# Kernel optimization log

Hardware: AMD Instinct MI355X
Metric: run time of the kernel (lower is better)

## Reference

```python
import jax, jax.numpy as jnp
import numpy as np

N = 100000   # nodes
E = 1600000  # edges (avg degree 16)
D = 32       # feature / hidden dim


def setup_inputs() -> dict:
    key = jax.random.key(0)
    k_x, k_e, kq, kk, kv, ko = jax.random.split(key, 6)
    s = 1.0 / np.sqrt(D).astype(np.float32)
    x = jax.random.normal(k_x, (N, D), dtype=jnp.float32)
    edge_index = jax.random.randint(k_e, (2, E), 0, N, dtype=jnp.int64)
    Wq = jax.random.normal(kq, (D, D), dtype=jnp.float32) * s
    Wk = jax.random.normal(kk, (D, D), dtype=jnp.float32) * s
    Wv = jax.random.normal(kv, (D, D), dtype=jnp.float32) * s
    Wo = jax.random.normal(ko, (D, D), dtype=jnp.float32) * s
    return {"x": x, "edge_index": edge_index, "Wq": Wq, "Wk": Wk, "Wv": Wv, "Wo": Wo}


def reference(x, edge_index, Wq, Wk, Wv, Wo):
    sender, receiver = edge_index[0], edge_index[1]
    n = x.shape[0]
    scale = x.shape[1] ** -0.5  # hidden_dim == D
    Q = x @ Wq  # [N, D]
    K = x @ Wk
    V = x @ Wv
    # per-edge attention scores
    scores = jnp.sum(Q[receiver] * K[sender], axis=1) * scale  # [E]
    # numerically-stable segment softmax over incoming edges of each receiver
    smax = jax.ops.segment_max(scores, receiver, num_segments=n)  # [N]
    alpha = jnp.exp(scores - smax[receiver])  # [E]
    Z = jax.ops.segment_sum(alpha, receiver, num_segments=n)  # [N]
    alpha = alpha / (Z[receiver] + 1e-6)
    # weighted aggregation of sender values
    out = jax.ops.segment_sum(alpha[:, None] * V[sender], receiver, num_segments=n)  # [N, D]
    return x + out @ Wo
```

## Files before the change

kernel.cpp:

```cpp
#include <hip/hip_runtime.h>

#define DIM 32
#define RCR 256
#define NCMAX 1024
#define PBLK 256
#define SUBCAP 48
#define REGSZ (PBLK * SUBCAP)
#define CAPC 5248

__device__ __forceinline__ float b2f(ushort h) {
    union { float f; unsigned u; } u; u.u = ((unsigned)h) << 16; return u.f;
}
__device__ __forceinline__ float h2f(ushort u) {
    _Float16 h; __builtin_memcpy(&h, &u, 2); return (float)h;
}
__device__ __forceinline__ ushort f2h(float f) {
    _Float16 h = (_Float16)f; ushort u; __builtin_memcpy(&u, &h, 2); return u;
}
__device__ __forceinline__ int clampN(int v, int n) {
    return v < 0 ? 0 : (v >= n ? n - 1 : v);
}
__device__ __forceinline__ int load_idx(const int* __restrict__ idx, size_t pos,
                                        int mode, int n) {
    int v = mode ? idx[2 * pos] : idx[pos];
    return clampN(v, n);
}
__device__ __forceinline__ float load_f(const void* p, size_t i, int bf) {
    return bf ? b2f(((const ushort*)p)[i]) : ((const float*)p)[i];
}

typedef _Float16 half2v __attribute__((ext_vector_type(2)));
__device__ __forceinline__ float dot2(unsigned a, unsigned b, float c) {
#if __has_builtin(__builtin_amdgcn_fdot2)
    half2v ha, hb;
    __builtin_memcpy(&ha, &a, 4); __builtin_memcpy(&hb, &b, 4);
    return __builtin_amdgcn_fdot2(ha, hb, c, false);
#else
    return fmaf(h2f((ushort)(a >> 16)), h2f((ushort)(b >> 16)),
                fmaf(h2f((ushort)a), h2f((ushort)b), c));
#endif
}

union K1Smem {
    struct { float sW[3][DIM * DIM]; float sx[32][36]; } g;
    struct { int h[NCMAX]; } place;
};

__global__ void __launch_bounds__(256)
qkv_place_kernel(const void* __restrict__ x_, const int* __restrict__ idx,
                 const void* __restrict__ Wq_, const void* __restrict__ Wk_,
                 const void* __restrict__ Wv_, int N, int E, int nc,
                 ushort* __restrict__ Q, ushort* __restrict__ KV,
                 unsigned* __restrict__ bedges, int* __restrict__ hcnt) {
    __shared__ K1Smem sm;
    __shared__ int sBf, sMode;

    const int tid = threadIdx.x;
    if (tid < 64) {
        int e = (((const ushort*)x_)[2 * tid] >> 7) & 0xFF;
        unsigned long long bb = __ballot(e >= 100 && e <= 135);
        unsigned long long mm = __ballot(idx[2 * tid + 1] != 0);
        if (tid == 0) { sBf = (__popcll(bb) >= 56); sMode = (mm == 0ULL); }
    }
    __syncthreads();
    const int bf = sBf, mode = sMode;

    if (blockIdx.x < PBLK) {
        const int pb = blockIdx.x;
        for (int i = tid; i < nc; i += 256) sm.place.h[i] = 0;
        __syncthreads();
        const int per = (E + PBLK - 1) / PBLK;
        const int e0 = pb * per;
        const int e1 = min(e0 + per, E);
        for (int e = e0 + tid; e < e1; e += 256) {
            const int r = load_idx(idx, (size_t)E + e, mode, N);
            const int s = load_idx(idx, (size_t)e, mode, N);
            const int reg = r >> 8;
            const int rl  = r & (RCR - 1);
            const int p = atomicAdd(&sm.place.h[reg], 1);
            if (p < SUBCAP)
                bedges[(size_t)reg * REGSZ + pb * SUBCAP + p] =
                    (unsigned)s | ((unsigned)rl << 17);
        }
        __syncthreads();
        for (int i = tid; i < nc; i += 256)
            hcnt[i * PBLK + pb] = min(sm.place.h[i], SUBCAP);
        return;
    }

    for (int i = tid; i < DIM * DIM; i += 256) {
        sm.g.sW[0][i] = load_f(Wq_, i, bf);
        sm.g.sW[1][i] = load_f(Wk_, i, bf);
        sm.g.sW[2][i] = load_f(Wv_, i, bf);
    }
    const int base = (blockIdx.x - PBLK) * 32;
    for (int i = tid; i < 32 * 8; i += 256) {
        const int r  = i >> 3;
        const int c4 = (i & 7) << 2;
        const int row = base + r;
        float4 v; v.x = v.y = v.z = v.w = 0.f;
        if (row < N) {
            if (!bf) {
                v = *(const float4*)((const float*)x_ + (size_t)row * DIM + c4);
            } else {
                const ushort4 u =
                    *(const ushort4*)((const ushort*)x_ + (size_t)row * DIM + c4);
                v.x = b2f(u.x); v.y = b2f(u.y); v.z = b2f(u.z); v.w = b2f(u.w);
            }
        }
        *(float4*)&sm.g.sx[r][c4] = v;
    }
    __syncthreads();

    const int lr  = tid >> 3;
    const int d4  = (tid & 7) << 2;
    const int row = base + lr;
    if (row >= N) return;

    float aq[4] = {0.f, 0.f, 0.f, 0.f};
    float ak[4] = {0.f, 0.f, 0.f, 0.f};
    float av[4] = {0.f, 0.f, 0.f, 0.f};
#pragma unroll
    for (int k0 = 0; k0 < DIM; k0 += 4) {
        const float4 xq = *(const float4*)&sm.g.sx[lr][k0];
        const float xs[4] = {xq.x, xq.y, xq.z, xq.w};
#pragma unroll
        for (int kk = 0; kk < 4; ++kk) {
            const float xv = xs[kk];
            const float4 wq = *(const float4*)&sm.g.sW[0][(k0 + kk) * DIM + d4];
            const float4 wk = *(const float4*)&sm.g.sW[1][(k0 + kk) * DIM + d4];
            const float4 wv = *(const float4*)&sm.g.sW[2][(k0 + kk) * DIM + d4];
            aq[0] = fmaf(xv, wq.x, aq[0]); aq[1] = fmaf(xv, wq.y, aq[1]);
            aq[2] = fmaf(xv, wq.z, aq[2]); aq[3] = fmaf(xv, wq.w, aq[3]);
            ak[0] = fmaf(xv, wk.x, ak[0]); ak[1] = fmaf(xv, wk.y, ak[1]);
            ak[2] = fmaf(xv, wk.z, ak[2]); ak[3] = fmaf(xv, wk.w, ak[3]);
            av[0] = fmaf(xv, wv.x, av[0]); av[1] = fmaf(xv, wv.y, av[1]);
            av[2] = fmaf(xv, wv.z, av[2]); av[3] = fmaf(xv, wv.w, av[3]);
        }
    }
    const float sc = 0.17677669529663687f;
    ushort4 t;
    t.x = f2h(aq[0] * sc); t.y = f2h(aq[1] * sc);
    t.z = f2h(aq[2] * sc); t.w = f2h(aq[3] * sc);
    *(ushort4*)&Q[(size_t)row * DIM + d4] = t;
    t.x = f2h(ak[0]); t.y = f2h(ak[1]); t.z = f2h(ak[2]); t.w = f2h(ak[3]);
    *(ushort4*)&KV[(size_t)row * 64 + d4] = t;
    t.x = f2h(av[0]); t.y = f2h(av[1]); t.z = f2h(av[2]); t.w = f2h(av[3]);
    *(ushort4*)&KV[(size_t)row * 64 + 32 + d4] = t;
}

__global__ void __launch_bounds__(512)
rsort_kernel(unsigned* __restrict__ bedges, const int* __restrict__ hcnt,
             int* __restrict__ rbase, int* __restrict__ rcount, int N) {
    __shared__ unsigned eL[CAPC];
    __shared__ int cnt[RCR];
    __shared__ int fills[PBLK];
    __shared__ int cbase[PBLK];
    __shared__ int wsum[4];

    const int tid = threadIdx.x;
    const int c = blockIdx.x;
    const size_t s0 = (size_t)c * REGSZ;
    const int lane = tid & 63, w = tid >> 6;

    if (tid < RCR) cnt[tid] = 0;
    if (tid < PBLK) fills[tid] = hcnt[c * PBLK + tid];
    __syncthreads();

    int fv = 0, fx = 0;
    if (tid < PBLK) {
        fv = fills[tid]; fx = fv;
#pragma unroll
        for (int o = 1; o < 64; o <<= 1) {
            int t = __shfl_up(fx, o); if (lane >= o) fx += t;
        }
        if (lane == 63) wsum[w] = fx;
    }
    __syncthreads();
    if (tid == 0) {
        int a = 0;
#pragma unroll
        for (int k = 0; k < 4; ++k) { int t = wsum[k]; wsum[k] = a; a += t; }
    }
    __syncthreads();
    if (tid < PBLK) cbase[tid] = fx - fv + wsum[w];
    __syncthreads();
    const int nTot = cbase[PBLK - 1] + fills[PBLK - 1];

    for (int j = tid; j < REGSZ / 4; j += 512) {
        const int cell = j / (SUBCAP / 4);
        const int q0   = (j - cell * (SUBCAP / 4)) * 4;
        const int fc   = fills[cell];
        if (q0 < fc) {
            const uint4 e4 = *(const uint4*)&bedges[s0 + (size_t)j * 4];
            const int base = cbase[cell] + q0;
            if (base < CAPC) {
                eL[base] = e4.x;
                atomicAdd(&cnt[(e4.x >> 17) & (RCR - 1)], 1);
            }
            if (q0 + 1 < fc && base + 1 < CAPC) {
                eL[base + 1] = e4.y;
                atomicAdd(&cnt[(e4.y >> 17) & (RCR - 1)], 1);
            }
            if (q0 + 2 < fc && base + 2 < CAPC) {
                eL[base + 2] = e4.z;
                atomicAdd(&cnt[(e4.z >> 17) & (RCR - 1)], 1);
            }
            if (q0 + 3 < fc && base + 3 < CAPC) {
                eL[base + 3] = e4.w;
                atomicAdd(&cnt[(e4.w >> 17) & (RCR - 1)], 1);
            }
        }
    }
    __syncthreads();

    const int v = (tid < RCR) ? cnt[tid] : 0;
    int x = v;
    if (tid < RCR) {
#pragma unroll
        for (int o = 1; o < 64; o <<= 1) {
            int t = __shfl_up(x, o); if (lane >= o) x += t;
        }
        if (lane == 63) wsum[w] = x;
    }
    __syncthreads();
    if (tid == 0) {
        int a = 0;
#pragma unroll
        for (int k = 0; k < 4; ++k) { int t = wsum[k]; wsum[k] = a; a += t; }
    }
    __syncthreads();
    int excl = 0;
    if (tid < RCR) {
        excl = x - v + wsum[w];
        rbase[c * RCR + tid]  = (int)s0 + excl;
        rcount[c * RCR + tid] = v;
    }
    __syncthreads();
    if (tid < RCR) cnt[tid] = excl;
    __syncthreads();

    const int m = min(nTot, CAPC);
    for (int i = tid; i < m; i += 512) {
        const unsigned e = eL[i];
        const int p = atomicAdd(&cnt[(e >> 17) & (RCR - 1)], 1);
        bedges[s0 + p] = e & 0x1FFFF;
    }
}

__global__ void __launch_bounds__(256)
agg_kernel(const ushort* __restrict__ Q, const ushort* __restrict__ KV,
           const unsigned* __restrict__ bedges, const int* __restrict__ rbase,
           const int* __restrict__ rcount, const void* __restrict__ x_,
           const void* __restrict__ Wo_, int N, float* __restrict__ out) {
    __shared__ float sWo[DIM * DIM];
    __shared__ float accS[32][DIM + 1];
    __shared__ float Zs[32];
    __shared__ unsigned sQ[32 * 16];
    __shared__ int sBf;

    const int tid = threadIdx.x;
    if (tid < 64) {
        int e = (((const ushort*)x_)[2 * tid] >> 7) & 0xFF;
        unsigned long long bb = __ballot(e >= 100 && e <= 135);
        if (tid == 0) sBf = (__popcll(bb) >= 56);
    }
    const int r0 = blockIdx.x * 32;
    const int nr = min(32, N - r0);
    __syncthreads();
    const int bf = sBf;

    for (int i = tid; i < DIM * DIM; i += 256) sWo[i] = load_f(Wo_, i, bf);
    for (int i = tid; i < nr * 16; i += 256)
        sQ[i] = ((const unsigned*)(Q + (size_t)r0 * DIM))[i];
    __syncthreads();

    const int w    = tid >> 6;
    const int lane = tid & 63;
    const int i8   = lane >> 3;
    const int j    = lane & 7;

    for (int t = w; t < nr; t += 8) {
        const int rlA = t;
        const int rlB = t + 4;
        const bool hasB = (rlB < nr);

        const int degA = rcount[r0 + rlA];
        const int o0A  = rbase[r0 + rlA];
        const int degB = hasB ? rcount[r0 + rlB] : 0;
        const int o0B  = hasB ? rbase[r0 + rlB] : o0A;

        const unsigned qA01 = sQ[rlA * 16 + j * 2];
        const unsigned qA23 = sQ[rlA * 16 + j * 2 + 1];
        const unsigned qB01 = sQ[(rlB & 31) * 16 + j * 2];
        const unsigned qB23 = sQ[(rlB & 31) * 16 + j * 2 + 1];

        float axA = 0.f, ayA = 0.f, azA = 0.f, awA = 0.f, zsA = 0.f;
        float axB = 0.f, ayB = 0.f, azB = 0.f, awB = 0.f, zsB = 0.f;

        const int chA = (degA + 7) >> 3;
        const int chB = (degB + 7) >> 3;
        const int cmax = max(chA, chB);
        const int dmA = max(degA - 1, 0);
        const int dmB = max(degB - 1, 0);

        for (int cc = 0; cc < cmax; cc += 2) {
            const int c0 = cc * 8 + i8;
            const int c1 = c0 + 8;
            const bool okA0 = (c0 < degA), okA1 = (c1 < degA);
            const bool okB0 = (c0 < degB), okB1 = (c1 < degB);

            const int sA0 = (int)bedges[o0A + (okA0 ? c0 : dmA)];
            const int sA1 = (int)bedges[o0A + (okA1 ? c1 : dmA)];
            const int sB0 = (int)bedges[o0B + (okB0 ? c0 : dmB)];
            const int sB1 = (int)bedges[o0B + (okB1 ? c1 : dmB)];

            const ushort* pA0 = KV + (size_t)sA0 * 64;
            const ushort* pA1 = KV + (size_t)sA1 * 64;
            const ushort* pB0 = KV + (size_t)sB0 * 64;
            const ushort* pB1 = KV + (size_t)sB1 * 64;

            const uint2 kA0 = *(const uint2*)(pA0 + j * 4);
            const uint2 vA0 = *(const uint2*)(pA0 + 32 + j * 4);
            const uint2 kA1 = *(const uint2*)(pA1 + j * 4);
            const uint2 vA1 = *(const uint2*)(pA1 + 32 + j * 4);
            const uint2 kB0 = *(const uint2*)(pB0 + j * 4);
            const uint2 vB0 = *(const uint2*)(pB0 + 32 + j * 4);
            const uint2 kB1 = *(const uint2*)(pB1 + j * 4);
            const uint2 vB1 = *(const uint2*)(pB1 + 32 + j * 4);

            float pA  = dot2(kA0.y, qA23, dot2(kA0.x, qA01, 0.f));
            float pAx = dot2(kA1.y, qA23, dot2(kA1.x, qA01, 0.f));
            float pB  = dot2(kB0.y, qB23, dot2(kB0.x, qB01, 0.f));
            float pBx = dot2(kB1.y, qB23, dot2(kB1.x, qB01, 0.f));

            pA  += __shfl_xor(pA, 1);   pAx += __shfl_xor(pAx, 1);
            pB  += __shfl_xor(pB, 1);   pBx += __shfl_xor(pBx, 1);
            pA  += __shfl_xor(pA, 2);   pAx += __shfl_xor(pAx, 2);
            pB  += __shfl_xor(pB, 2);   pBx += __shfl_xor(pBx, 2);
            pA  += __shfl_xor(pA, 4);   pAx += __shfl_xor(pAx, 4);
            pB  += __shfl_xor(pB, 4);   pBx += __shfl_xor(pBx, 4);

            pA  = fminf(fmaxf(pA,  -60.f), 60.f);
            pAx = fminf(fmaxf(pAx, -60.f), 60.f);
            pB  = fminf(fmaxf(pB,  -60.f), 60.f);
            pBx = fminf(fmaxf(pBx, -60.f), 60.f);
            const float aA0 = okA0 ? __expf(pA)  : 0.f;
            const float aA1 = okA1 ? __expf(pAx) : 0.f;
            const float aB0 = okB0 ? __expf(pB)  : 0.f;
            const float aB1 = okB1 ? __expf(pBx) : 0.f;

            axA = fmaf(h2f((ushort)vA0.x), aA0, axA);
            ayA = fmaf(h2f((ushort)(vA0.x >> 16)), aA0, ayA);
            azA = fmaf(h2f((ushort)vA0.y), aA0, azA);
            awA = fmaf(h2f((ushort)(vA0.y >> 16)), aA0, awA);
            axA = fmaf(h2f((ushort)vA1.x), aA1, axA);
            ayA = fmaf(h2f((ushort)(vA1.x >> 16)), aA1, ayA);
            azA = fmaf(h2f((ushort)vA1.y), aA1, azA);
            awA = fmaf(h2f((ushort)(vA1.y >> 16)), aA1, awA);
            zsA += aA0 + aA1;

            axB = fmaf(h2f((ushort)vB0.x), aB0, axB);
            ayB = fmaf(h2f((ushort)(vB0.x >> 16)), aB0, ayB);
            azB = fmaf(h2f((ushort)vB0.y), aB0, azB);
            awB = fmaf(h2f((ushort)(vB0.y >> 16)), aB0, awB);
            axB = fmaf(h2f((ushort)vB1.x), aB1, axB);
            ayB = fmaf(h2f((ushort)(vB1.x >> 16)), aB1, ayB);
            azB = fmaf(h2f((ushort)vB1.y), aB1, azB);
            awB = fmaf(h2f((ushort)(vB1.y >> 16)), aB1, awB);
            zsB += aB0 + aB1;
        }

#pragma unroll
        for (int o = 8; o < 64; o <<= 1) {
            axA += __shfl_xor(axA, o); ayA += __shfl_xor(ayA, o);
            azA += __shfl_xor(azA, o); awA += __shfl_xor(awA, o);
            zsA += __shfl_xor(zsA, o);
            axB += __shfl_xor(axB, o); ayB += __shfl_xor(ayB, o);
            azB += __shfl_xor(azB, o); awB += __shfl_xor(awB, o);
            zsB += __shfl_xor(zsB, o);
        }
        if (i8 == 0) {
            float* arA = accS[rlA];
            arA[j * 4 + 0] = axA; arA[j * 4 + 1] = ayA;
            arA[j * 4 + 2] = azA; arA[j * 4 + 3] = awA;
            if (j == 0) Zs[rlA] = zsA;
            if (hasB) {
                float* arB = accS[rlB];
                arB[j * 4 + 0] = axB; arB[j * 4 + 1] = ayB;
                arB[j * 4 + 2] = azB; arB[j * 4 + 3] = awB;
                if (j == 0) Zs[rlB] = zsB;
            }
        }
    }
    __syncthreads();

    const int lr = tid >> 5;
    const int d  = tid & 31;
#pragma unroll
    for (int it = 0; it < 4; ++it) {
        const int rl = it * 8 + lr;
        if (rl < nr) {
            const float inv = 1.f / (Zs[rl] + 1e-6f);
            float o = 0.f;
#pragma unroll
            for (int k = 0; k < DIM; ++k) o += accS[rl][k] * sWo[k * DIM + d];
            const size_t oi = (size_t)(r0 + rl) * DIM + d;
            out[oi] = load_f(x_, oi, bf) + inv * o;
        }
    }
}

extern "C" void kernel_launch(void* const* d_in, const int* in_sizes, int n_in,
                              void* d_out, int out_size, void* d_ws, size_t ws_size,
                              hipStream_t stream) {
    const void* x   = d_in[0];
    const int*  idx = (const int*)d_in[1];
    const void* Wq  = d_in[2];
    const void* Wk  = d_in[3];
    const void* Wv  = d_in[4];
    const void* Wo  = d_in[5];
    float* out = (float*)d_out;

    const int N = in_sizes[0] / DIM;
    const int E = in_sizes[1] / 2;
    const int nc = (N + RCR - 1) / RCR;
    const size_t N32 = (size_t)N * DIM;

    ushort*   Q      = (ushort*)d_ws;
    ushort*   KV     = Q + N32;
    unsigned* bedges = (unsigned*)(KV + (size_t)N * 64);
    int*      hcnt   = (int*)(bedges + (size_t)nc * REGSZ);
    int*      rbase  = hcnt + (size_t)nc * PBLK;
    int*      rcount = rbase + (size_t)nc * RCR;

    const int gemm_blocks = (N + 31) / 32;
    qkv_place_kernel<<<PBLK + gemm_blocks, 256, 0, stream>>>(
        x, idx, Wq, Wk, Wv, N, E, nc, Q, KV, bedges, hcnt);

    rsort_kernel<<<nc, 512, 0, stream>>>(bedges, hcnt, rbase, rcount, N);

    agg_kernel<<<(N + 31) / 32, 256, 0, stream>>>(Q, KV, bedges, rbase,
                                                  rcount, x, Wo, N, out);
}
```

Measured before the change: 177.1 us.

## Gather 16-byte K/V chunks with four lanes per edge, four rows per wave

Restructures the per-receiver gather loop. Each edge now uses 4 lanes doing 16-byte loads instead of 8 lanes doing 8-byte loads, so 16 edges are processed per wave step. Each wave handles four receiver rows at once over two passes instead of two. This widens the memory transactions and raises the number of independent gathers in flight. In exchange it adds more registers for the 32 accumulators plus the q vectors, and the final cross-lane reduction grows from 10 to 36 values per step.

```diff
diff --git a/kernel.cpp b/kernel.cpp
--- a/kernel.cpp
+++ b/kernel.cpp
@@ -277,119 +277,89 @@
 
     const int w    = tid >> 6;
     const int lane = tid & 63;
-    const int i8   = lane >> 3;
-    const int j    = lane & 7;
-
-    for (int t = w; t < nr; t += 8) {
-        const int rlA = t;
-        const int rlB = t + 4;
-        const bool hasB = (rlB < nr);
-
-        const int degA = rcount[r0 + rlA];
-        const int o0A  = rbase[r0 + rlA];
-        const int degB = hasB ? rcount[r0 + rlB] : 0;
-        const int o0B  = hasB ? rbase[r0 + rlB] : o0A;
-
-        const unsigned qA01 = sQ[rlA * 16 + j * 2];
-        const unsigned qA23 = sQ[rlA * 16 + j * 2 + 1];
-        const unsigned qB01 = sQ[(rlB & 31) * 16 + j * 2];
-        const unsigned qB23 = sQ[(rlB & 31) * 16 + j * 2 + 1];
-
-        float axA = 0.f, ayA = 0.f, azA = 0.f, awA = 0.f, zsA = 0.f;
-        float axB = 0.f, ayB = 0.f, azB = 0.f, awB = 0.f, zsB = 0.f;
-
-        const int chA = (degA + 7) >> 3;
-        const int chB = (degB + 7) >> 3;
-        const int cmax = max(chA, chB);
-        const int dmA = max(degA - 1, 0);
-        const int dmB = max(degB - 1, 0);
-
-        for (int cc = 0; cc < cmax; cc += 2) {
-            const int c0 = cc * 8 + i8;
-            const int c1 = c0 + 8;
-            const bool okA0 = (c0 < degA), okA1 = (c1 < degA);
-            const bool okB0 = (c0 < degB), okB1 = (c1 < degB);
-
-            const int sA0 = (int)bedges[o0A + (okA0 ? c0 : dmA)];
-            const int sA1 = (int)bedges[o0A + (okA1 ? c1 : dmA)];
-            const int sB0 = (int)bedges[o0B + (okB0 ? c0 : dmB)];
-            const int sB1 = (int)bedges[o0B + (okB1 ? c1 : dmB)];
-
-            const ushort* pA0 = KV + (size_t)sA0 * 64;
-            const ushort* pA1 = KV + (size_t)sA1 * 64;
-            const ushort* pB0 = KV + (size_t)sB0 * 64;
-            const ushort* pB1 = KV + (size_t)sB1 * 64;
-
-            const uint2 kA0 = *(const uint2*)(pA0 + j * 4);
-            const uint2 vA0 = *(const uint2*)(pA0 + 32 + j * 4);
-            const uint2 kA1 = *(const uint2*)(pA1 + j * 4);
-            const uint2 vA1 = *(const uint2*)(pA1 + 32 + j * 4);
-            const uint2 kB0 = *(const uint2*)(pB0 + j * 4);
-            const uint2 vB0 = *(const uint2*)(pB0 + 32 + j * 4);
-            const uint2 kB1 = *(const uint2*)(pB1 + j * 4);
-            const uint2 vB1 = *(const uint2*)(pB1 + 32 + j * 4);
-
-            float pA  = dot2(kA0.y, qA23, dot2(kA0.x, qA01, 0.f));
-            float pAx = dot2(kA1.y, qA23, dot2(kA1.x, qA01, 0.f));
-            float pB  = dot2(kB0.y, qB23, dot2(kB0.x, qB01, 0.f));
-            float pBx = dot2(kB1.y, qB23, dot2(kB1.x, qB01, 0.f));
-
-            pA  += __shfl_xor(pA, 1);   pAx += __shfl_xor(pAx, 1);
-            pB  += __shfl_xor(pB, 1);   pBx += __shfl_xor(pBx, 1);
-            pA  += __shfl_xor(pA, 2);   pAx += __shfl_xor(pAx, 2);
-            pB  += __shfl_xor(pB, 2);   pBx += __shfl_xor(pBx, 2);
-            pA  += __shfl_xor(pA, 4);   pAx += __shfl_xor(pAx, 4);
-            pB  += __shfl_xor(pB, 4);   pBx += __shfl_xor(pBx, 4);
-
-            pA  = fminf(fmaxf(pA,  -60.f), 60.f);
-            pAx = fminf(fmaxf(pAx, -60.f), 60.f);
-            pB  = fminf(fmaxf(pB,  -60.f), 60.f);
-            pBx = fminf(fmaxf(pBx, -60.f), 60.f);
-            const float aA0 = okA0 ? __expf(pA)  : 0.f;
-            const float aA1 = okA1 ? __expf(pAx) : 0.f;
-            const float aB0 = okB0 ? __expf(pB)  : 0.f;
-            const float aB1 = okB1 ? __expf(pBx) : 0.f;
-
-            axA = fmaf(h2f((ushort)vA0.x), aA0, axA);
-            ayA = fmaf(h2f((ushort)(vA0.x >> 16)), aA0, ayA);
-            azA = fmaf(h2f((ushort)vA0.y), aA0, azA);
-            awA = fmaf(h2f((ushort)(vA0.y >> 16)), aA0, awA);
-            axA = fmaf(h2f((ushort)vA1.x), aA1, axA);
-            ayA = fmaf(h2f((ushort)(vA1.x >> 16)), aA1, ayA);
-            azA = fmaf(h2f((ushort)vA1.y), aA1, azA);
-            awA = fmaf(h2f((ushort)(vA1.y >> 16)), aA1, awA);
-            zsA += aA0 + aA1;
-
-            axB = fmaf(h2f((ushort)vB0.x), aB0, axB);
-            ayB = fmaf(h2f((ushort)(vB0.x >> 16)), aB0, ayB);
-            azB = fmaf(h2f((ushort)vB0.y), aB0, azB);
-            awB = fmaf(h2f((ushort)(vB0.y >> 16)), aB0, awB);
-            axB = fmaf(h2f((ushort)vB1.x), aB1, axB);
-            ayB = fmaf(h2f((ushort)(vB1.x >> 16)), aB1, ayB);
-            azB = fmaf(h2f((ushort)vB1.y), aB1, azB);
-            awB = fmaf(h2f((ushort)(vB1.y >> 16)), aB1, awB);
-            zsB += aB0 + aB1;
-        }
-
-#pragma unroll
-        for (int o = 8; o < 64; o <<= 1) {
-            axA += __shfl_xor(axA, o); ayA += __shfl_xor(ayA, o);
-            azA += __shfl_xor(azA, o); awA += __shfl_xor(awA, o);
-            zsA += __shfl_xor(zsA, o);
-            axB += __shfl_xor(axB, o); ayB += __shfl_xor(ayB, o);
-            azB += __shfl_xor(azB, o); awB += __shfl_xor(awB, o);
-            zsB += __shfl_xor(zsB, o);
-        }
-        if (i8 == 0) {
-            float* arA = accS[rlA];
-            arA[j * 4 + 0] = axA; arA[j * 4 + 1] = ayA;
-            arA[j * 4 + 2] = azA; arA[j * 4 + 3] = awA;
-            if (j == 0) Zs[rlA] = zsA;
-            if (hasB) {
-                float* arB = accS[rlB];
-                arB[j * 4 + 0] = axB; arB[j * 4 + 1] = ayB;
-                arB[j * 4 + 2] = azB; arB[j * 4 + 3] = awB;
-                if (j == 0) Zs[rlB] = zsB;
+    const int i16  = lane >> 2;
+    const int j    = lane & 3;
+
+    for (int qq = 0; qq < 2; ++qq) {
+        int rl[4], deg[4], o0[4], dm[4];
+        uint4 qw[4];
+        float acc[4][8];
+        float zs[4];
+#pragma unroll
+        for (int k = 0; k < 4; ++k) {
+            rl[k] = w + 4 * k + 16 * qq;
+            const bool valid = rl[k] < nr;
+            deg[k] = valid ? rcount[r0 + rl[k]] : 0;
+            o0[k]  = valid ? rbase[r0 + rl[k]] : rbase[r0];
+            dm[k]  = max(deg[k] - 1, 0);
+            qw[k]  = ((const uint4*)(sQ + (rl[k] & 31) * 16))[j];
+#pragma unroll
+            for (int i = 0; i < 8; ++i) acc[k][i] = 0.f;
+            zs[k] = 0.f;
+        }
+        const int cmax = max(max((deg[0] + 15) >> 4, (deg[1] + 15) >> 4),
+                             max((deg[2] + 15) >> 4, (deg[3] + 15) >> 4));
+
+        for (int cc = 0; cc < cmax; ++cc) {
+            const int c0 = cc * 16 + i16;
+            bool ok[4]; int sx[4];
+#pragma unroll
+            for (int k = 0; k < 4; ++k) {
+                ok[k] = c0 < deg[k];
+                sx[k] = (int)bedges[o0[k] + (ok[k] ? c0 : dm[k])];
+            }
+            uint4 kw[4], vw[4];
+#pragma unroll
+            for (int k = 0; k < 4; ++k) {
+                const ushort* p = KV + (size_t)sx[k] * 64;
+                kw[k] = *(const uint4*)(p + j * 8);
+                vw[k] = *(const uint4*)(p + 32 + j * 8);
+            }
+            float a[4];
+#pragma unroll
+            for (int k = 0; k < 4; ++k) {
+                float p = dot2(kw[k].x, qw[k].x, 0.f);
+                p = dot2(kw[k].y, qw[k].y, p);
+                p = dot2(kw[k].z, qw[k].z, p);
+                p = dot2(kw[k].w, qw[k].w, p);
+                p += __shfl_xor(p, 1);
+                p += __shfl_xor(p, 2);
+                p = fminf(fmaxf(p, -60.f), 60.f);
+                a[k] = ok[k] ? __expf(p) : 0.f;
+            }
+#pragma unroll
+            for (int k = 0; k < 4; ++k) {
+                acc[k][0] = fmaf(h2f((ushort)vw[k].x),         a[k], acc[k][0]);
+                acc[k][1] = fmaf(h2f((ushort)(vw[k].x >> 16)), a[k], acc[k][1]);
+                acc[k][2] = fmaf(h2f((ushort)vw[k].y),         a[k], acc[k][2]);
+                acc[k][3] = fmaf(h2f((ushort)(vw[k].y >> 16)), a[k], acc[k][3]);
+                acc[k][4] = fmaf(h2f((ushort)vw[k].z),         a[k], acc[k][4]);
+                acc[k][5] = fmaf(h2f((ushort)(vw[k].z >> 16)), a[k], acc[k][5]);
+                acc[k][6] = fmaf(h2f((ushort)vw[k].w),         a[k], acc[k][6]);
+                acc[k][7] = fmaf(h2f((ushort)(vw[k].w >> 16)), a[k], acc[k][7]);
+                zs[k] += a[k];
+            }
+        }
+
+#pragma unroll
+        for (int o = 4; o < 64; o <<= 1) {
+#pragma unroll
+            for (int k = 0; k < 4; ++k) {
+#pragma unroll
+                for (int i = 0; i < 8; ++i)
+                    acc[k][i] += __shfl_xor(acc[k][i], o);
+                zs[k] += __shfl_xor(zs[k], o);
+            }
+        }
+        if (i16 == 0) {
+#pragma unroll
+            for (int k = 0; k < 4; ++k) {
+                if (rl[k] < nr) {
+#pragma unroll
+                    for (int i = 0; i < 8; ++i)
+                        accS[rl[k]][j * 8 + i] = acc[k][i];
+                    if (j == 0) Zs[rl[k]] = zs[k];
+                }
             }
         }
     }
```

Measured after the change: 198.0 us. +11.8%, slower.

## Move QKV GEMM from place kernel into rsort kernel and vectorize index loads

Applied to the files above, without the earlier changes.

Splits edge placement into its own kernel with 512 threads, loading two edges per iteration through vectorized int2/int4 loads. The QKV projection moves out of the placement kernel and runs alongside the per-region sort in a combined launch, using 64-row tiles at 512 threads. The aim is to shorten the placement phase and fill the otherwise under-occupied sort launch (only a few hundred blocks) with GEMM work. The cost is a larger shared-memory union that may limit occupancy, plus a different block mix per launch.

```diff
diff --git a/kernel.cpp b/kernel.cpp
--- a/kernel.cpp
+++ b/kernel.cpp
@@ -41,62 +41,205 @@
 #endif
 }
 
-union K1Smem {
-    struct { float sW[3][DIM * DIM]; float sx[32][36]; } g;
-    struct { int h[NCMAX]; } place;
-};
-
-__global__ void __launch_bounds__(256)
-qkv_place_kernel(const void* __restrict__ x_, const int* __restrict__ idx,
-                 const void* __restrict__ Wq_, const void* __restrict__ Wk_,
-                 const void* __restrict__ Wv_, int N, int E, int nc,
-                 ushort* __restrict__ Q, ushort* __restrict__ KV,
-                 unsigned* __restrict__ bedges, int* __restrict__ hcnt) {
-    __shared__ K1Smem sm;
-    __shared__ int sBf, sMode;
+__global__ void __launch_bounds__(512)
+place_kernel(const int* __restrict__ idx, int N, int E, int nc,
+             unsigned* __restrict__ bedges, int* __restrict__ hcnt) {
+    __shared__ int sh[NCMAX];
+    __shared__ int sMode;
 
     const int tid = threadIdx.x;
     if (tid < 64) {
-        int e = (((const ushort*)x_)[2 * tid] >> 7) & 0xFF;
-        unsigned long long bb = __ballot(e >= 100 && e <= 135);
         unsigned long long mm = __ballot(idx[2 * tid + 1] != 0);
-        if (tid == 0) { sBf = (__popcll(bb) >= 56); sMode = (mm == 0ULL); }
-    }
-    __syncthreads();
-    const int bf = sBf, mode = sMode;
-
-    if (blockIdx.x < PBLK) {
-        const int pb = blockIdx.x;
-        for (int i = tid; i < nc; i += 256) sm.place.h[i] = 0;
-        __syncthreads();
+        if (tid == 0) sMode = (mm == 0ULL);
+    }
+    for (int i = tid; i < nc; i += 512) sh[i] = 0;
+    __syncthreads();
+    const int mode = sMode;
+    const int pb = blockIdx.x;
+
+    if ((E & 1) == 0) {
+        const int pairs = E >> 1;
+        const int per = (pairs + PBLK - 1) / PBLK;
+        const int p0 = pb * per;
+        const int p1 = min(p0 + per, pairs);
+        for (int p = p0 + tid; p < p1; p += 512) {
+            int sa, sb, ra, rb;
+            if (mode) {
+                const int4 sv = *(const int4*)&idx[(size_t)4 * p];
+                const int4 rv = *(const int4*)&idx[2 * (size_t)E + (size_t)4 * p];
+                sa = sv.x; sb = sv.z; ra = rv.x; rb = rv.z;
+            } else {
+                const int2 sv = *(const int2*)&idx[(size_t)2 * p];
+                const int2 rv = *(const int2*)&idx[(size_t)E + (size_t)2 * p];
+                sa = sv.x; sb = sv.y; ra = rv.x; rb = rv.y;
+            }
+            sa = clampN(sa, N); sb = clampN(sb, N);
+            ra = clampN(ra, N); rb = clampN(rb, N);
+            const int ga = ra >> 8, la = ra & (RCR - 1);
+            const int gb = rb >> 8, lb = rb & (RCR - 1);
+            const int pa = atomicAdd(&sh[ga], 1);
+            if (pa < SUBCAP)
+                bedges[(size_t)ga * REGSZ + pb * SUBCAP + pa] =
+                    (unsigned)sa | ((unsigned)la << 17);
+            const int pb2 = atomicAdd(&sh[gb], 1);
+            if (pb2 < SUBCAP)
+                bedges[(size_t)gb * REGSZ + pb * SUBCAP + pb2] =
+                    (unsigned)sb | ((unsigned)lb << 17);
+        }
+    } else {
         const int per = (E + PBLK - 1) / PBLK;
         const int e0 = pb * per;
         const int e1 = min(e0 + per, E);
-        for (int e = e0 + tid; e < e1; e += 256) {
+        for (int e = e0 + tid; e < e1; e += 512) {
             const int r = load_idx(idx, (size_t)E + e, mode, N);
             const int s = load_idx(idx, (size_t)e, mode, N);
             const int reg = r >> 8;
             const int rl  = r & (RCR - 1);
-            const int p = atomicAdd(&sm.place.h[reg], 1);
+            const int p = atomicAdd(&sh[reg], 1);
             if (p < SUBCAP)
                 bedges[(size_t)reg * REGSZ + pb * SUBCAP + p] =
                     (unsigned)s | ((unsigned)rl << 17);
         }
-        __syncthreads();
-        for (int i = tid; i < nc; i += 256)
-            hcnt[i * PBLK + pb] = min(sm.place.h[i], SUBCAP);
+    }
+    __syncthreads();
+    for (int i = tid; i < nc; i += 512)
+        hcnt[i * PBLK + pb] = min(sh[i], SUBCAP);
+}
+
+union K2Smem {
+    struct {
+        unsigned eL[CAPC];
+        int cnt[RCR];
+        int fills[PBLK];
+        int cbase[PBLK];
+        int wsum[4];
+    } s;
+    struct {
+        float sW[3][DIM * DIM];
+        float sx[64][36];
+    } g;
+};
+
+__global__ void __launch_bounds__(512)
+rsort_gemm_kernel(unsigned* __restrict__ bedges, const int* __restrict__ hcnt,
+                  int* __restrict__ rbase, int* __restrict__ rcount,
+                  const void* __restrict__ x_, const void* __restrict__ Wq_,
+                  const void* __restrict__ Wk_, const void* __restrict__ Wv_,
+                  int N, int nc,
+                  ushort* __restrict__ Q, ushort* __restrict__ KV) {
+    __shared__ K2Smem sm;
+    __shared__ int sBf;
+
+    const int tid = threadIdx.x;
+
+    if (blockIdx.x < nc) {
+        const int c = blockIdx.x;
+        const size_t s0 = (size_t)c * REGSZ;
+        const int lane = tid & 63, w = tid >> 6;
+
+        if (tid < RCR) sm.s.cnt[tid] = 0;
+        if (tid < PBLK) sm.s.fills[tid] = hcnt[c * PBLK + tid];
+        __syncthreads();
+
+        int fv = 0, fx = 0;
+        if (tid < PBLK) {
+            fv = sm.s.fills[tid]; fx = fv;
+#pragma unroll
+            for (int o = 1; o < 64; o <<= 1) {
+                int t = __shfl_up(fx, o); if (lane >= o) fx += t;
+            }
+            if (lane == 63) sm.s.wsum[w] = fx;
+        }
+        __syncthreads();
+        if (tid == 0) {
+            int a = 0;
+#pragma unroll
+            for (int k = 0; k < 4; ++k) { int t = sm.s.wsum[k]; sm.s.wsum[k] = a; a += t; }
+        }
+        __syncthreads();
+        if (tid < PBLK) sm.s.cbase[tid] = fx - fv + sm.s.wsum[w];
+        __syncthreads();
+        const int nTot = sm.s.cbase[PBLK - 1] + sm.s.fills[PBLK - 1];
+
+        for (int j = tid; j < REGSZ / 4; j += 512) {
+            const int cell = j / (SUBCAP / 4);
+            const int q0   = (j - cell * (SUBCAP / 4)) * 4;
+            const int fc   = sm.s.fills[cell];
+            if (q0 < fc) {
+                const uint4 e4 = *(const uint4*)&bedges[s0 + (size_t)j * 4];
+                const int base = sm.s.cbase[cell] + q0;
+                if (base < CAPC) {
+                    sm.s.eL[base] = e4.x;
+                    atomicAdd(&sm.s.cnt[(e4.x >> 17) & (RCR - 1)], 1);
+                }
+                if (q0 + 1 < fc && base + 1 < CAPC) {
+                    sm.s.eL[base + 1] = e4.y;
+                    atomicAdd(&sm.s.cnt[(e4.y >> 17) & (RCR - 1)], 1);
+                }
+                if (q0 + 2 < fc && base + 2 < CAPC) {
+                    sm.s.eL[base + 2] = e4.z;
+                    atomicAdd(&sm.s.cnt[(e4.z >> 17) & (RCR - 1)], 1);
+                }
+                if (q0 + 3 < fc && base + 3 < CAPC) {
+                    sm.s.eL[base + 3] = e4.w;
+                    atomicAdd(&sm.s.cnt[(e4.w >> 17) & (RCR - 1)], 1);
+                }
+            }
+        }
+        __syncthreads();
+
+        const int v = (tid < RCR) ? sm.s.cnt[tid] : 0;
+        int x = v;
+        if (tid < RCR) {
+#pragma unroll
+            for (int o = 1; o < 64; o <<= 1) {
+                int t = __shfl_up(x, o); if (lane >= o) x += t;
+            }
+            if (lane == 63) sm.s.wsum[w] = x;
+        }
+        __syncthreads();
+        if (tid == 0) {
+            int a = 0;
+#pragma unroll
+            for (int k = 0; k < 4; ++k) { int t = sm.s.wsum[k]; sm.s.wsum[k] = a; a += t; }
+        }
+        __syncthreads();
+        int excl = 0;
+        if (tid < RCR) {
+            excl = x - v + sm.s.wsum[w];
+            rbase[c * RCR + tid]  = (int)s0 + excl;
+            rcount[c * RCR + tid] = v;
+        }
+        __syncthreads();
+        if (tid < RCR) sm.s.cnt[tid] = excl;
+        __syncthreads();
+
+        const int m = min(nTot, CAPC);
+        for (int i = tid; i < m; i += 512) {
+            const unsigned e = sm.s.eL[i];
+            const int p = atomicAdd(&sm.s.cnt[(e >> 17) & (RCR - 1)], 1);
+            bedges[s0 + p] = e & 0x1FFFF;
+        }
         return;
     }
 
-    for (int i = tid; i < DIM * DIM; i += 256) {
+    if (tid < 64) {
+        int e = (((const ushort*)x_)[2 * tid] >> 7) & 0xFF;
+        unsigned long long bb = __ballot(e >= 100 && e <= 135);
+        if (tid == 0) sBf = (__popcll(bb) >= 56);
+    }
+    __syncthreads();
+    const int bf = sBf;
+
+    for (int i = tid; i < DIM * DIM; i += 512) {
         sm.g.sW[0][i] = load_f(Wq_, i, bf);
         sm.g.sW[1][i] = load_f(Wk_, i, bf);
         sm.g.sW[2][i] = load_f(Wv_, i, bf);
     }
-    const int base = (blockIdx.x - PBLK) * 32;
-    for (int i = tid; i < 32 * 8; i += 256) {
-        const int r  = i >> 3;
-        const int c4 = (i & 7) << 2;
+    const int base = (blockIdx.x - nc) * 64;
+    {
+        const int r  = tid >> 3;
+        const int c4 = (tid & 7) << 2;
         const int row = base + r;
         float4 v; v.x = v.y = v.z = v.w = 0.f;
         if (row < N) {
@@ -149,105 +292,6 @@
     *(ushort4*)&KV[(size_t)row * 64 + 32 + d4] = t;
 }
 
-__global__ void __launch_bounds__(512)
-rsort_kernel(unsigned* __restrict__ bedges, const int* __restrict__ hcnt,
-             int* __restrict__ rbase, int* __restrict__ rcount, int N) {
-    __shared__ unsigned eL[CAPC];
-    __shared__ int cnt[RCR];
-    __shared__ int fills[PBLK];
-    __shared__ int cbase[PBLK];
-    __shared__ int wsum[4];
-
-    const int tid = threadIdx.x;
-    const int c = blockIdx.x;
-    const size_t s0 = (size_t)c * REGSZ;
-    const int lane = tid & 63, w = tid >> 6;
-
-    if (tid < RCR) cnt[tid] = 0;
-    if (tid < PBLK) fills[tid] = hcnt[c * PBLK + tid];
-    __syncthreads();
-
-    int fv = 0, fx = 0;
-    if (tid < PBLK) {
-        fv = fills[tid]; fx = fv;
-#pragma unroll
-        for (int o = 1; o < 64; o <<= 1) {
-            int t = __shfl_up(fx, o); if (lane >= o) fx += t;
-        }
-        if (lane == 63) wsum[w] = fx;
-    }
-    __syncthreads();
-    if (tid == 0) {
-        int a = 0;
-#pragma unroll
-        for (int k = 0; k < 4; ++k) { int t = wsum[k]; wsum[k] = a; a += t; }
-    }
-    __syncthreads();
-    if (tid < PBLK) cbase[tid] = fx - fv + wsum[w];
-    __syncthreads();
-    const int nTot = cbase[PBLK - 1] + fills[PBLK - 1];
-
-    for (int j = tid; j < REGSZ / 4; j += 512) {
-        const int cell = j / (SUBCAP / 4);
-        const int q0   = (j - cell * (SUBCAP / 4)) * 4;
-        const int fc   = fills[cell];
-        if (q0 < fc) {
-            const uint4 e4 = *(const uint4*)&bedges[s0 + (size_t)j * 4];
-            const int base = cbase[cell] + q0;
-            if (base < CAPC) {
-                eL[base] = e4.x;
-                atomicAdd(&cnt[(e4.x >> 17) & (RCR - 1)], 1);
-            }
-            if (q0 + 1 < fc && base + 1 < CAPC) {
-                eL[base + 1] = e4.y;
-                atomicAdd(&cnt[(e4.y >> 17) & (RCR - 1)], 1);
-            }
-            if (q0 + 2 < fc && base + 2 < CAPC) {
-                eL[base + 2] = e4.z;
-                atomicAdd(&cnt[(e4.z >> 17) & (RCR - 1)], 1);
-            }
-            if (q0 + 3 < fc && base + 3 < CAPC) {
-                eL[base + 3] = e4.w;
-                atomicAdd(&cnt[(e4.w >> 17) & (RCR - 1)], 1);
-            }
-        }
-    }
-    __syncthreads();
-
-    const int v = (tid < RCR) ? cnt[tid] : 0;
-    int x = v;
-    if (tid < RCR) {
-#pragma unroll
-        for (int o = 1; o < 64; o <<= 1) {
-            int t = __shfl_up(x, o); if (lane >= o) x += t;
-        }
-        if (lane == 63) wsum[w] = x;
-    }
-    __syncthreads();
-    if (tid == 0) {
-        int a = 0;
-#pragma unroll
-        for (int k = 0; k < 4; ++k) { int t = wsum[k]; wsum[k] = a; a += t; }
-    }
-    __syncthreads();
-    int excl = 0;
-    if (tid < RCR) {
-        excl = x - v + wsum[w];
-        rbase[c * RCR + tid]  = (int)s0 + excl;
-        rcount[c * RCR + tid] = v;
-    }
-    __syncthreads();
-    if (tid < RCR) cnt[tid] = excl;
-    __syncthreads();
-
-    const int m = min(nTot, CAPC);
-    for (int i = tid; i < m; i += 512) {
-        const unsigned e = eL[i];
-        const int p = atomicAdd(&cnt[(e >> 17) & (RCR - 1)], 1);
-        bedges[s0 + p] = e & 0x1FFFF;
-    }
-}
-
 __global__ void __launch_bounds__(256)
 agg_kernel(const ushort* __restrict__ Q, const ushort* __restrict__ KV,
            const unsigned* __restrict__ bedges, const int* __restrict__ rbase,
@@ -434,11 +478,11 @@
     int*      rbase  = hcnt + (size_t)nc * PBLK;
     int*      rcount = rbase + (size_t)nc * RCR;
 
-    const int gemm_blocks = (N + 31) / 32;
-    qkv_place_kernel<<<PBLK + gemm_blocks, 256, 0, stream>>>(
-        x, idx, Wq, Wk, Wv, N, E, nc, Q, KV, bedges, hcnt);
-
-    rsort_kernel<<<nc, 512, 0, stream>>>(bedges, hcnt, rbase, rcount, N);
+    place_kernel<<<PBLK, 512, 0, stream>>>(idx, N, E, nc, bedges, hcnt);
+
+    const int gemm_blocks = (N + 63) / 64;
+    rsort_gemm_kernel<<<nc + gemm_blocks, 512, 0, stream>>>(
+        bedges, hcnt, rbase, rcount, x, Wq, Wk, Wv, N, nc, Q, KV);
 
     agg_kernel<<<(N + 31) / 32, 256, 0, stream>>>(Q, KV, bedges, rbase,
                                                   rcount, x, Wo, N, out);
```

After: 181.5 us. 1.02x slower.
